# Optimization experiments

Hardware: AMD Instinct MI355X
Metric: run time of the kernel (lower is better)

The kernel has to match this reference:

```python
import jax, jax.numpy as jnp
import numpy as np

EMBED = 2048
HEADS = 16
DHEAD = EMBED // HEADS


def setup_inputs() -> dict:
    key = jax.random.key(0)
    k1, k2, k3 = jax.random.split(key, 3)
    x = jax.random.normal(k1, (4, 2048, EMBED), dtype=jnp.float32)
    # torch Linear weight layout: [out_features, in_features]; y = x @ W.T
    W_in = jax.random.normal(k2, (3 * EMBED, EMBED), dtype=jnp.float32) * (EMBED ** -0.5)
    W_out = jax.random.normal(k3, (EMBED, EMBED), dtype=jnp.float32) * (EMBED ** -0.5)
    return {"x": x, "W_in": W_in, "W_out": W_out}


def reference(x, W_in, W_out):
    B, T, C = x.shape
    qkv = jnp.einsum('btc,fc->btf', x, W_in)          # [B,T,3C]
    q, k, v = jnp.split(qkv, 3, axis=-1)
    def heads(t):
        return t.reshape(B, T, HEADS, DHEAD).transpose(0, 2, 1, 3)  # [B,H,T,D]
    q, k, v = heads(q), heads(k), heads(v)
    scale = DHEAD ** -0.5
    scores = jnp.einsum('bhtd,bhsd->bhts', q, k) * scale  # [B,H,T,T]
    causal = jnp.tril(jnp.ones((T, T), dtype=bool))
    scores = jnp.where(causal, scores, jnp.finfo(scores.dtype).min)
    attn = jax.nn.softmax(scores, axis=-1)
    y = jnp.einsum('bhts,bhsd->bhtd', attn, v)            # [B,H,T,D]
    y = y.transpose(0, 2, 1, 3).reshape(B, T, C)
    return jnp.einsum('btc,fc->btf', y, W_out)
```

## Files before the change

### kernel.cpp

```cpp
#include <hip/hip_runtime.h>

typedef unsigned short u16;
typedef unsigned int u32;
typedef __attribute__((ext_vector_type(8))) short bf16x8;
typedef __attribute__((ext_vector_type(4))) float f32x4;
typedef __attribute__((ext_vector_type(8))) unsigned short u16x8;
typedef __attribute__((ext_vector_type(4))) unsigned short u16x4;
typedef __attribute__((ext_vector_type(4))) u32 u32x4;

#define MFMA16 __builtin_amdgcn_mfma_f32_16x16x32_bf16

__device__ __forceinline__ u16 f2bf(float f) {
  unsigned u = __float_as_uint(f);
  u += 0x7fffu + ((u >> 16) & 1u);
  return (u16)(u >> 16);
}

__device__ __forceinline__ void async16(void* lds, const void* g) {
  __builtin_amdgcn_global_load_lds(
      (const __attribute__((address_space(1))) unsigned int*)g,
      (__attribute__((address_space(3))) unsigned int*)lds, 16, 0, 0);
}

__global__ void convert_bf16(const float* __restrict__ in, u16* __restrict__ out, int n4) {
  int i = blockIdx.x * blockDim.x + threadIdx.x;
  int st = gridDim.x * blockDim.x;
  for (; i < n4; i += st) {
    float4 f = ((const float4*)in)[i];
    ushort4 o;
    o.x = f2bf(f.x); o.y = f2bf(f.y); o.z = f2bf(f.z); o.w = f2bf(f.w);
    ((ushort4*)out)[i] = o;
  }
}

#define GEMM256_CORE(A_, B_)                                                    \
  __shared__ __align__(16) char lds[131072];                                    \
  const int tid = threadIdx.x;                                                  \
  const int lane = tid & 63, w = tid >> 6;                                      \
  const int wr = w >> 2, wc = w & 3;                                            \
  const int fr = lane & 15, fq = lane >> 4;                                     \
  const int lrA = tid >> 3, ccA = tid & 7, w8 = w << 3;                         \
  f32x4 acc[8][4] = {};                                                         \
  const u16* Abase = A_ + (size_t)tm * 2048;                                    \
  const u16* Bbase = B_ + (size_t)tn * 2048;                                    \
  auto stageA = [&](int mh, int kt, char* buf) {                                \
    _Pragma("unroll") for (int it = 0; it < 2; ++it) {                          \
      int lrt = it * 64 + lrA;                                                  \
      int row = mh * 64 + (lrt & 63) + ((lrt & 64) << 1);                       \
      const u16* src = Abase + (size_t)row * 2048 + kt + ((ccA ^ (row & 7)) << 3); \
      int lr0 = it * 64 + w8;                                                   \
      int row0 = mh * 64 + (lr0 & 63) + ((lr0 & 64) << 1);                      \
      async16(buf + row0 * 128, src);                                           \
    }                                                                           \
  };                                                                            \
  auto stageB = [&](int nh, int kt, char* buf) {                                \
    _Pragma("unroll") for (int it = 0; it < 2; ++it) {                          \
      int lrt = it * 64 + lrA;                                                  \
      int nr = ((lrt >> 5) << 6) + nh * 32 + (lrt & 31);                        \
      const u16* src = Bbase + (size_t)nr * 2048 + kt + ((ccA ^ (nr & 7)) << 3); \
      int lr0 = it * 64 + w8;                                                   \
      int nr0 = ((lr0 >> 5) << 6) + nh * 32 + (lr0 & 31);                       \
      async16(buf + 32768 + nr0 * 128, src);                                    \
    }                                                                           \
  };                                                                            \
  stageA(0, 0, lds); stageB(0, 0, lds); stageB(1, 0, lds); stageA(1, 0, lds);   \
  for (int t = 0; t < 32; ++t) {                                                \
    char* cur = lds + (t & 1) * 65536;                                          \
    char* nxt = lds + ((t + 1) & 1) * 65536;                                    \
    const int ktn = (t + 1) * 64;                                               \
    const bool more = (t + 1 < 32);                                             \
                                                        \
    asm volatile("s_waitcnt vmcnt(2)" ::: "memory");                            \
    __builtin_amdgcn_s_barrier();                                               \
    asm volatile("" ::: "memory");                                              \
    bf16x8 af[4][2], bfr[4][2];                                                 \
    _Pragma("unroll") for (int i = 0; i < 4; ++i) {                             \
      int rr = wr * 128 + i * 16 + fr;                                          \
      _Pragma("unroll") for (int ks = 0; ks < 2; ++ks)                          \
        af[i][ks] = *(const bf16x8*)(cur + rr * 128 +                           \
                                     (((ks * 4 + fq) ^ (rr & 7)) << 4));        \
    }                                                                           \
    _Pragma("unroll") for (int j = 0; j < 4; ++j) {                             \
      int nr = wc * 64 + j * 16 + fr;                                           \
      _Pragma("unroll") for (int ks = 0; ks < 2; ++ks)                          \
        bfr[j][ks] = *(const bf16x8*)(cur + 32768 + nr * 128 +                  \
                                      (((ks * 4 + fq) ^ (nr & 7)) << 4));       \
    }                                                                           \
    if (more) { stageA(0, ktn, nxt); stageB(0, ktn, nxt); }                     \
    __builtin_amdgcn_s_setprio(1);                                              \
    _Pragma("unroll") for (int ks = 0; ks < 2; ++ks)                            \
      _Pragma("unroll") for (int i = 0; i < 4; ++i)                             \
        _Pragma("unroll") for (int j = 0; j < 4; ++j)                           \
          acc[i][j] = MFMA16(af[i][ks], bfr[j][ks], acc[i][j], 0, 0, 0);        \
    __builtin_amdgcn_s_setprio(0);                                              \
                                                        \
    if (more) asm volatile("s_waitcnt vmcnt(4)" ::: "memory");                  \
    else      asm volatile("s_waitcnt vmcnt(0)" ::: "memory");                  \
    __builtin_amdgcn_s_barrier();                                               \
    asm volatile("" ::: "memory");                                              \
    bf16x8 ag[4][2];                                                            \
    _Pragma("unroll") for (int i = 0; i < 4; ++i) {                             \
      int rr = wr * 128 + 64 + i * 16 + fr;                                     \
      _Pragma("unroll") for (int ks = 0; ks < 2; ++ks)                          \
        ag[i][ks] = *(const bf16x8*)(cur + rr * 128 +                           \
                                     (((ks * 4 + fq) ^ (rr & 7)) << 4));        \
    }                                                                           \
    if (more) { stageB(1, ktn, nxt); stageA(1, ktn, nxt); }                     \
    __builtin_amdgcn_s_setprio(1);                                              \
    _Pragma("unroll") for (int ks = 0; ks < 2; ++ks)                            \
      _Pragma("unroll") for (int i = 0; i < 4; ++i)                             \
        _Pragma("unroll") for (int j = 0; j < 4; ++j)                           \
          acc[4 + i][j] = MFMA16(ag[i][ks], bfr[j][ks], acc[4 + i][j], 0, 0, 0);\
    __builtin_amdgcn_s_setprio(0);                                              \
  }

__global__ __launch_bounds__(512, 2) void gemm_qkv8(
    const u16* __restrict__ A, const u16* __restrict__ B,
    u16* __restrict__ Qb, u16* __restrict__ Kb, u16* __restrict__ Vtb) {
  int id = blockIdx.x;
  int swz = (id & 7) * 96 + (id >> 3);
  const int tm = (swz / 24) * 256, tn = (swz % 24) * 256;
  GEMM256_CORE(A, B)
#pragma unroll
  for (int J = 0; J < 4; ++J) {
    int n = tn + wc * 64 + J * 16 + fr;
    int which = n >> 11, h = (n >> 7) & 15, d = n & 127;
    if (which < 2) {
      u16* dst = which == 0 ? Qb : Kb;
#pragma unroll
      for (int I = 0; I < 8; ++I)
#pragma unroll
        for (int rr = 0; rr < 4; ++rr) {
          int m = tm + wr * 128 + I * 16 + fq * 4 + rr;
          int bb = m >> 11, tt = m & 2047;
          dst[((size_t)((bb * 16 + h) * 2048 + tt) << 7) + d] = f2bf(acc[I][J][rr]);
        }
    } else {
#pragma unroll
      for (int I = 0; I < 8; ++I) {
        int m0 = tm + wr * 128 + I * 16 + fq * 4;
        int bb = m0 >> 11, tt0 = m0 & 2047;
        u16x4 pk;
#pragma unroll
        for (int rr = 0; rr < 4; ++rr) pk[rr] = f2bf(acc[I][J][rr]);
        *(u16x4*)&Vtb[(size_t)(bb * 16 + h) * 262144 + (size_t)d * 2048 + tt0] = pk;
      }
    }
  }
}

__global__ __launch_bounds__(512, 2) void gemm_out8(
    const u16* __restrict__ A, const u16* __restrict__ B, float* __restrict__ C) {
  int id = blockIdx.x;
  int swz = (id & 7) * 32 + (id >> 3);
  const int tm = (swz / 8) * 256, tn = (swz % 8) * 256;
  GEMM256_CORE(A, B)
#pragma unroll
  for (int J = 0; J < 4; ++J) {
    int n = tn + wc * 64 + J * 16 + fr;
#pragma unroll
    for (int I = 0; I < 8; ++I)
#pragma unroll
      for (int rr = 0; rr < 4; ++rr) {
        int m = tm + wr * 128 + I * 16 + fq * 4 + rr;
        C[(size_t)m * 2048 + n] = acc[I][J][rr];
      }
  }
}

__global__ __launch_bounds__(512, 4) void attn8(
    const u16* __restrict__ Q, const u16* __restrict__ K,
    const u16* __restrict__ Vt, u16* __restrict__ Y) {
  __shared__ __align__(16) char smem[49152];
  char* lK = smem;
  char* lV = smem + 16384;
  char* lP = smem + 32768;
  const int tid = threadIdx.x;
  const int lane = tid & 63, w = tid >> 6;
  const int fr = lane & 15, fq = lane >> 4;
  const int pair = blockIdx.x, by = blockIdx.y;
  const size_t hoff = (size_t)pair * 262144;
  const u16* Qh = Q + hoff;
  const u16* Kh = K + hoff;
  const u16* Vth = Vt + hoff;
  const int b = pair >> 4, h = pair & 15;
  const float c1 = 0.08838834764831845f * 1.4426950408889634f;
  const float THR = 11.5f;

  int ksr[2], kcc[2], vdr[2], vcc[2];
#pragma unroll
  for (int it = 0; it < 2; ++it) {
    int idx = it * 512 + tid;
    ksr[it] = idx >> 4; kcc[it] = idx & 15;
    vdr[it] = idx >> 3; vcc[it] = idx & 7;
  }

  for (int phase = 0; phase < 2; ++phase) {
    const int qb = phase ? 15 - by : by;
    const int q0 = qb * 128;
    const int nt = 2 * qb + 2;
    const int qw = q0 + w * 16;

    bf16x8 qf[4];
#pragma unroll
    for (int ks = 0; ks < 4; ++ks)
      qf[ks] = *(const bf16x8*)&Qh[(size_t)(qw + fr) * 128 + ks * 32 + fq * 8];

    f32x4 o[8] = {};
    float m2[4], ls[4];
#pragma unroll
    for (int r = 0; r < 4; ++r) { m2[r] = -1e30f; ls[r] = 0.f; }

    u32x4 kst[2], vst[2];
#pragma unroll
    for (int it = 0; it < 2; ++it) {
      kst[it] = *(const u32x4*)&Kh[(size_t)ksr[it] * 128 + kcc[it] * 8];
      vst[it] = *(const u32x4*)&Vth[(size_t)vdr[it] * 2048 + vcc[it] * 8];
    }

    for (int t = 0; t < nt; ++t) {
      const int kv0 = t * 64;
#pragma unroll
      for (int it = 0; it < 2; ++it) {
        *(u32x4*)(lK + ksr[it] * 256 + ((kcc[it] ^ (ksr[it] & 7)) << 4)) = kst[it];
        *(u32x4*)(lV + vdr[it] * 128 + ((vcc[it] ^ (vdr[it] & 7)) << 4)) = vst[it];
      }
      if (t + 1 < nt) {
        const int nk = kv0 + 64;
#pragma unroll
        for (int it = 0; it < 2; ++it) {
          kst[it] = *(const u32x4*)&Kh[(size_t)(nk + ksr[it]) * 128 + kcc[it] * 8];
          vst[it] = *(const u32x4*)&Vth[(size_t)vdr[it] * 2048 + nk + vcc[it] * 8];
        }
      }
      __syncthreads();

      if (kv0 <= qw + 15) {
        f32x4 sc[4] = {};
#pragma unroll
        for (int j = 0; j < 4; ++j) {
          int s = j * 16 + fr;
#pragma unroll
          for (int ks = 0; ks < 4; ++ks) {
            bf16x8 kf = *(const bf16x8*)(lK + s * 256 + (((ks * 32 + fq * 8) * 2) ^ ((s & 7) << 4)));
            sc[j] = MFMA16(qf[ks], kf, sc[j], 0, 0, 0);
          }
        }
        if (kv0 + 64 > qw) {
          int rowb = qw + fq * 4;
#pragma unroll
          for (int j = 0; j < 4; ++j) {
            int col = kv0 + j * 16 + fr;
#pragma unroll
            for (int r = 0; r < 4; ++r)
              if (col > rowb + r) sc[j][r] = -3e38f;
          }
        }
        float lmax[4];
        bool trip = false;
#pragma unroll
        for (int r = 0; r < 4; ++r) {
          lmax[r] = fmaxf(fmaxf(sc[0][r], sc[1][r]), fmaxf(sc[2][r], sc[3][r]));
          trip = trip || (lmax[r] * c1 > m2[r] + THR);
        }
        if (__any(trip)) {
#pragma unroll
          for (int r = 0; r < 4; ++r) {
            float v = lmax[r];
            v = fmaxf(v, __shfl_xor(v, 1));
            v = fmaxf(v, __shfl_xor(v, 2));
            v = fmaxf(v, __shfl_xor(v, 4));
            v = fmaxf(v, __shfl_xor(v, 8));
            v *= c1;
            float mn = fmaxf(m2[r], v);
            float corr = __builtin_amdgcn_exp2f(m2[r] - mn);
            m2[r] = mn;
            ls[r] *= corr;
#pragma unroll
            for (int n = 0; n < 8; ++n) o[n][r] *= corr;
          }
        }
#pragma unroll
        for (int r = 0; r < 4; ++r) {
          int prow = w * 16 + fq * 4 + r;
          float rs = 0.f;
#pragma unroll
          for (int j = 0; j < 4; ++j) {
            float p = __builtin_amdgcn_exp2f(sc[j][r] * c1 - m2[r]);
            rs += p;
            *(u16*)(lP + prow * 128 + (((j * 16 + fr) * 2) ^ ((prow & 7) << 4))) = f2bf(p);
          }
          ls[r] += rs;
        }
        bf16x8 pf[2];
        {
          int prow = w * 16 + fr;
#pragma unroll
          for (int k2 = 0; k2 < 2; ++k2)
            pf[k2] = *(const bf16x8*)(lP + prow * 128 + ((k2 * 64 + fq * 16) ^ ((prow & 7) << 4)));
        }
#pragma unroll
        for (int n = 0; n < 8; ++n) {
          int d = n * 16 + fr;
#pragma unroll
          for (int k2 = 0; k2 < 2; ++k2) {
            bf16x8 vf = *(const bf16x8*)(lV + d * 128 + ((k2 * 64 + fq * 16) ^ ((d & 7) << 4)));
            o[n] = MFMA16(pf[k2], vf, o[n], 0, 0, 0);
          }
        }
      }
      __syncthreads();
    }

    float inv[4];
#pragma unroll
    for (int r = 0; r < 4; ++r) {
      float s = ls[r];
      s += __shfl_xor(s, 1);
      s += __shfl_xor(s, 2);
      s += __shfl_xor(s, 4);
      s += __shfl_xor(s, 8);
      inv[r] = 1.f / s;
    }
#pragma unroll
    for (int n = 0; n < 8; ++n)
#pragma unroll
      for (int r = 0; r < 4; ++r) {
        int tt = qw + fq * 4 + r;
        Y[((size_t)(b * 2048 + tt) * 2048) + h * 128 + n * 16 + fr] = f2bf(o[n][r] * inv[r]);
      }
  }
}

extern "C" void kernel_launch(void* const* d_in, const int* in_sizes, int n_in,
                              void* d_out, int out_size, void* d_ws, size_t ws_size,
                              hipStream_t stream) {
  const float* x = (const float*)d_in[0];
  const float* Win = (const float*)d_in[1];
  const float* Wout = (const float*)d_in[2];
  float* out = (float*)d_out;
  char* ws = (char*)d_ws;

  u16* x_bf   = (u16*)(ws);
  u16* win_bf = (u16*)(ws + 33554432);
  u16* wout_bf= (u16*)(ws + 58720256);
  u16* Qb     = (u16*)(ws + 67108864);
  u16* Kb     = (u16*)(ws + 100663296);
  u16* Vtb    = (u16*)(ws + 134217728);
  u16* y_bf   = (u16*)(ws + 167772160);

  convert_bf16<<<2048, 256, 0, stream>>>(x, x_bf, 16777216 / 4);
  convert_bf16<<<2048, 256, 0, stream>>>(Win, win_bf, 12582912 / 4);
  convert_bf16<<<1024, 256, 0, stream>>>(Wout, wout_bf, 4194304 / 4);

  gemm_qkv8<<<768, 512, 0, stream>>>(x_bf, win_bf, Qb, Kb, Vtb);
  attn8<<<dim3(64, 8), 512, 0, stream>>>(Qb, Kb, Vtb, y_bf);
  gemm_out8<<<256, 512, 0, stream>>>(y_bf, wout_bf, out);
}
```

Before: 504.3 us.

## Restructure attention to 32x32 MFMA with register-resident P fragments

The attention kernel moves from 16x16x32 to 32x32x16 bf16 MFMA tiles, with 4 waves of 32 query rows each instead of 8 waves of 16. S is computed transposed (K as the A operand), so each lane holds one query column. Softmax row statistics then become per-lane scalars, and P is packed to bf16 and exchanged across half-waves with shuffles, which removes the LDS round trip for P. Block size drops to 256 threads and LDS to 32KB, trading more registers per wave for fewer LDS accesses and fewer shuffle reductions.

```diff
diff --git a/kernel.cpp b/kernel.cpp
--- a/kernel.cpp
+++ b/kernel.cpp
@@ -4,16 +4,24 @@
 typedef unsigned int u32;
 typedef __attribute__((ext_vector_type(8))) short bf16x8;
 typedef __attribute__((ext_vector_type(4))) float f32x4;
+typedef __attribute__((ext_vector_type(16))) float f32x16;
 typedef __attribute__((ext_vector_type(8))) unsigned short u16x8;
 typedef __attribute__((ext_vector_type(4))) unsigned short u16x4;
 typedef __attribute__((ext_vector_type(4))) u32 u32x4;
 
 #define MFMA16 __builtin_amdgcn_mfma_f32_16x16x32_bf16
+#define MFMA32 __builtin_amdgcn_mfma_f32_32x32x16_bf16
 
 __device__ __forceinline__ u16 f2bf(float f) {
   unsigned u = __float_as_uint(f);
   u += 0x7fffu + ((u >> 16) & 1u);
   return (u16)(u >> 16);
+}
+
+__device__ __forceinline__ u32 cvtpk(float lo, float hi) {
+  u32 r;
+  asm("v_cvt_pk_bf16_f32 %0, %1, %2" : "=v"(r) : "v"(lo), "v"(hi));
+  return r;
 }
 
 __device__ __forceinline__ void async16(void* lds, const void* g) {
@@ -69,7 +77,6 @@
     char* nxt = lds + ((t + 1) & 1) * 65536;                                    \
     const int ktn = (t + 1) * 64;                                               \
     const bool more = (t + 1 < 32);                                             \
-                                                        \
     asm volatile("s_waitcnt vmcnt(2)" ::: "memory");                            \
     __builtin_amdgcn_s_barrier();                                               \
     asm volatile("" ::: "memory");                                              \
@@ -93,7 +100,6 @@
         _Pragma("unroll") for (int j = 0; j < 4; ++j)                           \
           acc[i][j] = MFMA16(af[i][ks], bfr[j][ks], acc[i][j], 0, 0, 0);        \
     __builtin_amdgcn_s_setprio(0);                                              \
-                                                        \
     if (more) asm volatile("s_waitcnt vmcnt(4)" ::: "memory");                  \
     else      asm volatile("s_waitcnt vmcnt(0)" ::: "memory");                  \
     __builtin_amdgcn_s_barrier();                                               \
@@ -168,16 +174,15 @@
   }
 }
 
-__global__ __launch_bounds__(512, 4) void attn8(
+__global__ __launch_bounds__(256, 3) void attn13(
     const u16* __restrict__ Q, const u16* __restrict__ K,
     const u16* __restrict__ Vt, u16* __restrict__ Y) {
-  __shared__ __align__(16) char smem[49152];
+  __shared__ __align__(16) char smem[32768];
   char* lK = smem;
   char* lV = smem + 16384;
-  char* lP = smem + 32768;
   const int tid = threadIdx.x;
   const int lane = tid & 63, w = tid >> 6;
-  const int fr = lane & 15, fq = lane >> 4;
+  const int q32 = lane & 31, hi = lane >> 5;
   const int pair = blockIdx.x, by = blockIdx.y;
   const size_t hoff = (size_t)pair * 262144;
   const u16* Qh = Q + hoff;
@@ -187,10 +192,10 @@
   const float c1 = 0.08838834764831845f * 1.4426950408889634f;
   const float THR = 11.5f;
 
-  int ksr[2], kcc[2], vdr[2], vcc[2];
-#pragma unroll
-  for (int it = 0; it < 2; ++it) {
-    int idx = it * 512 + tid;
+  int ksr[4], kcc[4], vdr[4], vcc[4];
+#pragma unroll
+  for (int it = 0; it < 4; ++it) {
+    int idx = it * 256 + tid;
     ksr[it] = idx >> 4; kcc[it] = idx & 15;
     vdr[it] = idx >> 3; vcc[it] = idx & 7;
   }
@@ -199,21 +204,19 @@
     const int qb = phase ? 15 - by : by;
     const int q0 = qb * 128;
     const int nt = 2 * qb + 2;
-    const int qw = q0 + w * 16;
-
-    bf16x8 qf[4];
-#pragma unroll
-    for (int ks = 0; ks < 4; ++ks)
-      qf[ks] = *(const bf16x8*)&Qh[(size_t)(qw + fr) * 128 + ks * 32 + fq * 8];
-
-    f32x4 o[8] = {};
-    float m2[4], ls[4];
-#pragma unroll
-    for (int r = 0; r < 4; ++r) { m2[r] = -1e30f; ls[r] = 0.f; }
-
-    u32x4 kst[2], vst[2];
-#pragma unroll
-    for (int it = 0; it < 2; ++it) {
+    const int qw = q0 + w * 32;
+
+    bf16x8 qf[8];
+#pragma unroll
+    for (int ks = 0; ks < 8; ++ks)
+      qf[ks] = *(const bf16x8*)&Qh[(size_t)(qw + q32) * 128 + ks * 16 + hi * 8];
+
+    f32x16 o[4] = {};
+    float m2 = -1e30f, ls = 0.f;
+
+    u32x4 kst[4], vst[4];
+#pragma unroll
+    for (int it = 0; it < 4; ++it) {
       kst[it] = *(const u32x4*)&Kh[(size_t)ksr[it] * 128 + kcc[it] * 8];
       vst[it] = *(const u32x4*)&Vth[(size_t)vdr[it] * 2048 + vcc[it] * 8];
     }
@@ -221,114 +224,111 @@
     for (int t = 0; t < nt; ++t) {
       const int kv0 = t * 64;
 #pragma unroll
-      for (int it = 0; it < 2; ++it) {
-        *(u32x4*)(lK + ksr[it] * 256 + ((kcc[it] ^ (ksr[it] & 7)) << 4)) = kst[it];
+      for (int it = 0; it < 4; ++it) {
+        *(u32x4*)(lK + ksr[it] * 256 + ((kcc[it] ^ (ksr[it] & 15)) << 4)) = kst[it];
         *(u32x4*)(lV + vdr[it] * 128 + ((vcc[it] ^ (vdr[it] & 7)) << 4)) = vst[it];
       }
       if (t + 1 < nt) {
         const int nk = kv0 + 64;
 #pragma unroll
-        for (int it = 0; it < 2; ++it) {
+        for (int it = 0; it < 4; ++it) {
           kst[it] = *(const u32x4*)&Kh[(size_t)(nk + ksr[it]) * 128 + kcc[it] * 8];
           vst[it] = *(const u32x4*)&Vth[(size_t)vdr[it] * 2048 + nk + vcc[it] * 8];
         }
       }
       __syncthreads();
 
-      if (kv0 <= qw + 15) {
-        f32x4 sc[4] = {};
-#pragma unroll
-        for (int j = 0; j < 4; ++j) {
-          int s = j * 16 + fr;
-#pragma unroll
-          for (int ks = 0; ks < 4; ++ks) {
-            bf16x8 kf = *(const bf16x8*)(lK + s * 256 + (((ks * 32 + fq * 8) * 2) ^ ((s & 7) << 4)));
-            sc[j] = MFMA16(qf[ks], kf, sc[j], 0, 0, 0);
+      if (kv0 <= qw + 31) {
+        f32x16 sc[2] = {};
+#pragma unroll
+        for (int j = 0; j < 2; ++j) {
+          int s = j * 32 + q32;
+#pragma unroll
+          for (int ks = 0; ks < 8; ++ks) {
+            bf16x8 kf = *(const bf16x8*)(lK + s * 256 + (((ks * 2 + hi) ^ (s & 15)) << 4));
+            sc[j] = MFMA32(kf, qf[ks], sc[j], 0, 0, 0);
           }
         }
         if (kv0 + 64 > qw) {
-          int rowb = qw + fq * 4;
-#pragma unroll
-          for (int j = 0; j < 4; ++j) {
-            int col = kv0 + j * 16 + fr;
-#pragma unroll
-            for (int r = 0; r < 4; ++r)
-              if (col > rowb + r) sc[j][r] = -3e38f;
+#pragma unroll
+          for (int j = 0; j < 2; ++j)
+#pragma unroll
+            for (int rg = 0; rg < 16; ++rg) {
+              int kv = kv0 + j * 32 + (rg & 3) + 8 * (rg >> 2) + 4 * hi;
+              if (kv > qw + q32) sc[j][rg] = -3e38f;
+            }
+        }
+        float lmax = sc[0][0];
+#pragma unroll
+        for (int j = 0; j < 2; ++j)
+#pragma unroll
+          for (int rg = 0; rg < 16; ++rg) lmax = fmaxf(lmax, sc[j][rg]);
+        bool trip = lmax * c1 > m2 + THR;
+        if (__any(trip)) {
+          float v = fmaxf(lmax, __shfl_xor(lmax, 32)) * c1;
+          float mn = fmaxf(m2, v);
+          float corr = __builtin_amdgcn_exp2f(m2 - mn);
+          m2 = mn;
+          ls *= corr;
+#pragma unroll
+          for (int rg = 0; rg < 16; ++rg) {
+            float cr = __shfl(corr, (rg & 3) + 8 * (rg >> 2) + 4 * hi);
+#pragma unroll
+            for (int n = 0; n < 4; ++n) o[n][rg] *= cr;
           }
         }
-        float lmax[4];
-        bool trip = false;
-#pragma unroll
-        for (int r = 0; r < 4; ++r) {
-          lmax[r] = fmaxf(fmaxf(sc[0][r], sc[1][r]), fmaxf(sc[2][r], sc[3][r]));
-          trip = trip || (lmax[r] * c1 > m2[r] + THR);
-        }
-        if (__any(trip)) {
-#pragma unroll
-          for (int r = 0; r < 4; ++r) {
-            float v = lmax[r];
-            v = fmaxf(v, __shfl_xor(v, 1));
-            v = fmaxf(v, __shfl_xor(v, 2));
-            v = fmaxf(v, __shfl_xor(v, 4));
-            v = fmaxf(v, __shfl_xor(v, 8));
-            v *= c1;
-            float mn = fmaxf(m2[r], v);
-            float corr = __builtin_amdgcn_exp2f(m2[r] - mn);
-            m2[r] = mn;
-            ls[r] *= corr;
-#pragma unroll
-            for (int n = 0; n < 8; ++n) o[n][r] *= corr;
-          }
-        }
-#pragma unroll
-        for (int r = 0; r < 4; ++r) {
-          int prow = w * 16 + fq * 4 + r;
-          float rs = 0.f;
-#pragma unroll
-          for (int j = 0; j < 4; ++j) {
-            float p = __builtin_amdgcn_exp2f(sc[j][r] * c1 - m2[r]);
-            rs += p;
-            *(u16*)(lP + prow * 128 + (((j * 16 + fr) * 2) ^ ((prow & 7) << 4))) = f2bf(p);
-          }
-          ls[r] += rs;
-        }
-        bf16x8 pf[2];
-        {
-          int prow = w * 16 + fr;
-#pragma unroll
-          for (int k2 = 0; k2 < 2; ++k2)
-            pf[k2] = *(const bf16x8*)(lP + prow * 128 + ((k2 * 64 + fq * 16) ^ ((prow & 7) << 4)));
-        }
-#pragma unroll
-        for (int n = 0; n < 8; ++n) {
-          int d = n * 16 + fr;
-#pragma unroll
-          for (int k2 = 0; k2 < 2; ++k2) {
-            bf16x8 vf = *(const bf16x8*)(lV + d * 128 + ((k2 * 64 + fq * 16) ^ ((d & 7) << 4)));
-            o[n] = MFMA16(pf[k2], vf, o[n], 0, 0, 0);
+        float rs = 0.f;
+        bf16x8 pfrag[4];
+#pragma unroll
+        for (int st = 0; st < 4; ++st) {
+          const int j = st >> 1, rb = (st & 1) * 8;
+          float p0 = __builtin_amdgcn_exp2f(sc[j][rb + 0] * c1 - m2);
+          float p1 = __builtin_amdgcn_exp2f(sc[j][rb + 1] * c1 - m2);
+          float p2 = __builtin_amdgcn_exp2f(sc[j][rb + 2] * c1 - m2);
+          float p3 = __builtin_amdgcn_exp2f(sc[j][rb + 3] * c1 - m2);
+          float p4 = __builtin_amdgcn_exp2f(sc[j][rb + 4] * c1 - m2);
+          float p5 = __builtin_amdgcn_exp2f(sc[j][rb + 5] * c1 - m2);
+          float p6 = __builtin_amdgcn_exp2f(sc[j][rb + 6] * c1 - m2);
+          float p7 = __builtin_amdgcn_exp2f(sc[j][rb + 7] * c1 - m2);
+          rs += ((p0 + p1) + (p2 + p3)) + ((p4 + p5) + (p6 + p7));
+          u32 a  = cvtpk(p0, p1), a2 = cvtpk(p2, p3);
+          u32 bb_ = cvtpk(p4, p5), b2 = cvtpk(p6, p7);
+          u32 ax = (u32)__shfl_xor((int)a, 32);
+          u32 a2x = (u32)__shfl_xor((int)a2, 32);
+          u32 bx = (u32)__shfl_xor((int)bb_, 32);
+          u32 b2x = (u32)__shfl_xor((int)b2, 32);
+          union { u32 u[4]; bf16x8 v; } fw;
+          fw.u[0] = hi ? bx : a;
+          fw.u[1] = hi ? b2x : a2;
+          fw.u[2] = hi ? bb_ : ax;
+          fw.u[3] = hi ? b2 : a2x;
+          pfrag[st] = fw.v;
+        }
+        ls += rs;
+#pragma unroll
+        for (int n = 0; n < 4; ++n) {
+          int d = n * 32 + q32;
+#pragma unroll
+          for (int st = 0; st < 4; ++st) {
+            bf16x8 vf = *(const bf16x8*)(lV + d * 128 + (((st * 2 + hi) ^ (d & 7)) << 4));
+            o[n] = MFMA32(pfrag[st], vf, o[n], 0, 0, 0);
           }
         }
       }
       __syncthreads();
     }
 
-    float inv[4];
-#pragma unroll
-    for (int r = 0; r < 4; ++r) {
-      float s = ls[r];
-      s += __shfl_xor(s, 1);
-      s += __shfl_xor(s, 2);
-      s += __shfl_xor(s, 4);
-      s += __shfl_xor(s, 8);
-      inv[r] = 1.f / s;
+    float lst = ls + __shfl_xor(ls, 32);
+    float inv = 1.f / lst;
+#pragma unroll
+    for (int rg = 0; rg < 16; ++rg) {
+      int ql = (rg & 3) + 8 * (rg >> 2) + 4 * hi;
+      float iv = __shfl(inv, ql);
+      int trow = qw + ql;
+#pragma unroll
+      for (int n = 0; n < 4; ++n)
+        Y[(size_t)(b * 2048 + trow) * 2048 + h * 128 + n * 32 + q32] = f2bf(o[n][rg] * iv);
     }
-#pragma unroll
-    for (int n = 0; n < 8; ++n)
-#pragma unroll
-      for (int r = 0; r < 4; ++r) {
-        int tt = qw + fq * 4 + r;
-        Y[((size_t)(b * 2048 + tt) * 2048) + h * 128 + n * 16 + fr] = f2bf(o[n][r] * inv[r]);
-      }
   }
 }
 
@@ -354,6 +354,6 @@
   convert_bf16<<<1024, 256, 0, stream>>>(Wout, wout_bf, 4194304 / 4);
 
   gemm_qkv8<<<768, 512, 0, stream>>>(x_bf, win_bf, Qb, Kb, Vtb);
-  attn8<<<dim3(64, 8), 512, 0, stream>>>(Qb, Kb, Vtb, y_bf);
+  attn13<<<dim3(64, 8), 256, 0, stream>>>(Qb, Kb, Vtb, y_bf);
   gemm_out8<<<256, 512, 0, stream>>>(y_bf, wout_bf, out);
 }
```

After: 617.5 us. 22.4% more time.
